# Performance work log

Hardware: AMD Instinct MI355X
Metric: run time of the kernel (lower is better)

The kernel has to match this reference:

```python
import jax, jax.numpy as jnp
import numpy as np

WEIGHT_GROUP = 128  # in-channel group size for scales (module default)


def setup_inputs() -> dict:
    key = jax.random.key(0)
    k1, k2, k3, k4, k5 = jax.random.split(key, 5)
    B, IN, OUT = 16, 8192, 8192
    nG = IN // WEIGHT_GROUP  # 64 scale groups along in_features
    x = jax.random.normal(k1, (B, IN), dtype=jnp.float32)
    # 'weight' stores the already-quantized low-bit float values (small magnitudes)
    weight = jax.random.normal(k2, (OUT, IN), dtype=jnp.float32)
    # per-(row, group) positive scales
    scale_buf = jax.random.uniform(k3, (OUT, nG), dtype=jnp.float32, minval=0.01, maxval=1.0)
    bias = jax.random.normal(k4, (1, OUT), dtype=jnp.float32)
    # per-[64, group]-block mantissa-format ids in {0,1,2}; selects the dequant
    # format on hardware but is a constant lookup (no float math) in the reference
    types = jax.random.randint(k5, (OUT // 64, nG), 0, 3, dtype=jnp.int32)
    return {"x": x, "weight": weight, "scale_buf": scale_buf, "bias": bias, "types": types}


def reference(x, weight, scale_buf, bias, types):
    O, I = weight.shape
    nG = scale_buf.shape[1]
    G = I // nG
    # group-wise dequant: w_deq[o, g*G + j] = weight[o, g*G + j] * scale_buf[o, g]
    w_deq = (weight.reshape(O, nG, G) * scale_buf[:, :, None]).reshape(O, I)
    # y = x @ W_deq^T + bias   [B, O]
    return jnp.einsum("bi,oi->bo", x, w_deq) + bias
```

## Files before the change

### kernel.cpp

```cpp
#include <hip/hip_runtime.h>

#define IN_F 8192
#define OUT_F 8192
#define NBATCH 16
#define KC 512
#define NG 64
#define KSPLIT 2
#define KRANGE (IN_F / KSPLIT)

__global__ __launch_bounds__(256)
void init_out_kernel(const float* __restrict__ bias, float* __restrict__ out) {
    const int i = blockIdx.x * 256 + threadIdx.x;
    out[i] = bias[i & (OUT_F - 1)];
}

__global__ __launch_bounds__(256, 4)
void axcore_dsew_linear_kernel(const float* __restrict__ x,
                               const float* __restrict__ w,
                               const float* __restrict__ scale,
                               float* __restrict__ out) {
    __shared__ __align__(16) float xlds[NBATCH * KC];

    const int t    = threadIdx.x;
    const int wv   = __builtin_amdgcn_readfirstlane(t >> 6);
    const int lane = t & 63;
    const int o0   = blockIdx.x * 16 + wv * 4;
    const int k0   = blockIdx.y * KRANGE;

    float acc[4][NBATCH];
#pragma unroll
    for (int r = 0; r < 4; ++r)
#pragma unroll
        for (int b = 0; b < NBATCH; ++b) acc[r][b] = 0.f;

    for (int kc = k0; kc < k0 + KRANGE; kc += KC) {
        __syncthreads();

        float4 wq[2][4];
#pragma unroll
        for (int s = 0; s < 2; ++s)
#pragma unroll
            for (int r = 0; r < 4; ++r)
                wq[s][r] = *(const float4*)&w[(size_t)(o0 + r) * IN_F + kc + s * 256 + 4 * lane];

        const int g0 = kc >> 7;
        float sc[2][4];
#pragma unroll
        for (int s = 0; s < 2; ++s)
#pragma unroll
            for (int r = 0; r < 4; ++r) {
                const float sa = scale[(o0 + r) * NG + g0 + 2 * s];
                const float sb = scale[(o0 + r) * NG + g0 + 2 * s + 1];
                sc[s][r] = (lane < 32) ? sa : sb;
            }

#pragma unroll
        for (int p = 0; p < 8; ++p) {
            const int fidx = p * 256 + t;
            const int bb = fidx >> 7;
            const int kq = fidx & 127;
            *(float4*)&xlds[bb * KC + 4 * kq] =
                *(const float4*)&x[bb * IN_F + kc + 4 * kq];
        }
        __syncthreads();

#pragma unroll
        for (int s = 0; s < 2; ++s) {
            const int klocal = s * 256 + 4 * lane;
            float4 wr[4];
#pragma unroll
            for (int r = 0; r < 4; ++r) {
                wr[r].x = wq[s][r].x * sc[s][r];
                wr[r].y = wq[s][r].y * sc[s][r];
                wr[r].z = wq[s][r].z * sc[s][r];
                wr[r].w = wq[s][r].w * sc[s][r];
            }
#pragma unroll
            for (int b = 0; b < NBATCH; ++b) {
                const float4 xv = *(const float4*)&xlds[b * KC + klocal];
#pragma unroll
                for (int r = 0; r < 4; ++r) {
                    acc[r][b] += wr[r].x * xv.x;
                    acc[r][b] += wr[r].y * xv.y;
                    acc[r][b] += wr[r].z * xv.z;
                    acc[r][b] += wr[r].w * xv.w;
                }
            }
        }
    }

#pragma unroll
    for (int r = 0; r < 4; ++r) {
        const int o = o0 + r;
#pragma unroll
        for (int b = 0; b < NBATCH; ++b) {
            float v = acc[r][b];
            v += __shfl_xor(v, 1);
            v += __shfl_xor(v, 2);
            v += __shfl_xor(v, 4);
            v += __shfl_xor(v, 8);
            v += __shfl_xor(v, 16);
            v += __shfl_xor(v, 32);
            if (lane == 0) atomicAdd(&out[b * OUT_F + o], v);
        }
    }
}

extern "C" void kernel_launch(void* const* d_in, const int* in_sizes, int n_in,
                              void* d_out, int out_size, void* d_ws, size_t ws_size,
                              hipStream_t stream) {
    const float* x    = (const float*)d_in[0];
    const float* w    = (const float*)d_in[1];
    const float* sc   = (const float*)d_in[2];
    const float* bias = (const float*)d_in[3];
    float* out = (float*)d_out;

    hipLaunchKernelGGL(init_out_kernel, dim3(NBATCH * OUT_F / 256), dim3(256),
                       0, stream, bias, out);
    hipLaunchKernelGGL(axcore_dsew_linear_kernel, dim3(OUT_F / 16, KSPLIT), dim3(256),
                       0, stream, x, w, sc, out);
}
```

Baseline: 445.6 us.

## Use bf16 MFMA for dequantized GEMV with wider K-split

New measurement: 403.0 us. 9.6% less time.

```diff
diff --git a/kernel.cpp b/kernel.cpp
--- a/kernel.cpp
+++ b/kernel.cpp
@@ -1,12 +1,21 @@
 #include <hip/hip_runtime.h>
+#include <hip/hip_bf16.h>
 
 #define IN_F 8192
 #define OUT_F 8192
-#define NBATCH 16
-#define KC 512
+#define NB 16
 #define NG 64
-#define KSPLIT 2
+#define KSPLIT 8
 #define KRANGE (IN_F / KSPLIT)
+#define NSTEP (KRANGE / 32)
+
+typedef __attribute__((ext_vector_type(8))) short bf16x8;
+typedef __attribute__((ext_vector_type(4))) float f32x4;
+
+static __device__ __forceinline__ short f2bf(float f) {
+    __hip_bfloat16 h = __float2bfloat16(f);
+    return *reinterpret_cast<short*>(&h);
+}
 
 __global__ __launch_bounds__(256)
 void init_out_kernel(const float* __restrict__ bias, float* __restrict__ out) {
@@ -15,94 +24,77 @@
 }
 
 __global__ __launch_bounds__(256, 4)
-void axcore_dsew_linear_kernel(const float* __restrict__ x,
-                               const float* __restrict__ w,
-                               const float* __restrict__ scale,
-                               float* __restrict__ out) {
-    __shared__ __align__(16) float xlds[NBATCH * KC];
+void axcore_mfma_kernel(const float* __restrict__ x,
+                        const float* __restrict__ w,
+                        const float* __restrict__ scale,
+                        float* __restrict__ out) {
+    __shared__ __align__(16) unsigned short xswz[NSTEP * 64 * 8];
 
     const int t    = threadIdx.x;
-    const int wv   = __builtin_amdgcn_readfirstlane(t >> 6);
+    const int wv   = t >> 6;
     const int lane = t & 63;
-    const int o0   = blockIdx.x * 16 + wv * 4;
     const int k0   = blockIdx.y * KRANGE;
-
-    float acc[4][NBATCH];
-#pragma unroll
-    for (int r = 0; r < 4; ++r)
-#pragma unroll
-        for (int b = 0; b < NBATCH; ++b) acc[r][b] = 0.f;
-
-    for (int kc = k0; kc < k0 + KRANGE; kc += KC) {
-        __syncthreads();
-
-        float4 wq[2][4];
-#pragma unroll
-        for (int s = 0; s < 2; ++s)
-#pragma unroll
-            for (int r = 0; r < 4; ++r)
-                wq[s][r] = *(const float4*)&w[(size_t)(o0 + r) * IN_F + kc + s * 256 + 4 * lane];
-
-        const int g0 = kc >> 7;
-        float sc[2][4];
-#pragma unroll
-        for (int s = 0; s < 2; ++s)
-#pragma unroll
-            for (int r = 0; r < 4; ++r) {
-                const float sa = scale[(o0 + r) * NG + g0 + 2 * s];
-                const float sb = scale[(o0 + r) * NG + g0 + 2 * s + 1];
-                sc[s][r] = (lane < 32) ? sa : sb;
-            }
+    const int o0   = blockIdx.x * 64 + wv * 16;
 
 #pragma unroll
-        for (int p = 0; p < 8; ++p) {
-            const int fidx = p * 256 + t;
-            const int bb = fidx >> 7;
-            const int kq = fidx & 127;
-            *(float4*)&xlds[bb * KC + 4 * kq] =
-                *(const float4*)&x[bb * IN_F + kc + 4 * kq];
-        }
-        __syncthreads();
+    for (int p = 0; p < 16; ++p) {
+        const int idx = p * 256 + t;
+        const int m   = idx >> 8;
+        const int k4  = (idx & 255) * 4;
+        const float4 v = *(const float4*)&x[m * IN_F + k0 + k4];
+        const int tt = k4 >> 5;
+        const int ln = m + 16 * ((k4 & 31) >> 3);
+        const int jj = k4 & 7;
+        ushort4 sv;
+        sv.x = (unsigned short)f2bf(v.x);
+        sv.y = (unsigned short)f2bf(v.y);
+        sv.z = (unsigned short)f2bf(v.z);
+        sv.w = (unsigned short)f2bf(v.w);
+        *(ushort4*)&xswz[(tt * 64 + ln) * 8 + jj] = sv;
+    }
+    __syncthreads();
 
+    const int nrow = o0 + (lane & 15);
+    const int koct = (lane >> 4) * 8;
+    const float* wrow = &w[(size_t)nrow * IN_F];
+
+    const float4 sA = *(const float4*)&scale[nrow * NG + (k0 >> 7)];
+    const float4 sB = *(const float4*)&scale[nrow * NG + (k0 >> 7) + 4];
+    float sg[8] = {sA.x, sA.y, sA.z, sA.w, sB.x, sB.y, sB.z, sB.w};
+
+    f32x4 acc = {0.f, 0.f, 0.f, 0.f};
+
+#pragma unroll 2
+    for (int gi = 0; gi < KRANGE / 128; ++gi) {
+        const float s = sg[gi];
 #pragma unroll
-        for (int s = 0; s < 2; ++s) {
-            const int klocal = s * 256 + 4 * lane;
-            float4 wr[4];
-#pragma unroll
-            for (int r = 0; r < 4; ++r) {
-                wr[r].x = wq[s][r].x * sc[s][r];
-                wr[r].y = wq[s][r].y * sc[s][r];
-                wr[r].z = wq[s][r].z * sc[s][r];
-                wr[r].w = wq[s][r].w * sc[s][r];
-            }
-#pragma unroll
-            for (int b = 0; b < NBATCH; ++b) {
-                const float4 xv = *(const float4*)&xlds[b * KC + klocal];
-#pragma unroll
-                for (int r = 0; r < 4; ++r) {
-                    acc[r][b] += wr[r].x * xv.x;
-                    acc[r][b] += wr[r].y * xv.y;
-                    acc[r][b] += wr[r].z * xv.z;
-                    acc[r][b] += wr[r].w * xv.w;
-                }
-            }
+        for (int ts = 0; ts < 4; ++ts) {
+            const int tt = gi * 4 + ts;
+            const int kg = k0 + tt * 32 + koct;
+            const float4 w0 = *(const float4*)&wrow[kg];
+            const float4 w1 = *(const float4*)&wrow[kg + 4];
+
+            bf16x8 bfrag;
+            bfrag[0] = f2bf(w0.x * s);
+            bfrag[1] = f2bf(w0.y * s);
+            bfrag[2] = f2bf(w0.z * s);
+            bfrag[3] = f2bf(w0.w * s);
+            bfrag[4] = f2bf(w1.x * s);
+            bfrag[5] = f2bf(w1.y * s);
+            bfrag[6] = f2bf(w1.z * s);
+            bfrag[7] = f2bf(w1.w * s);
+
+            const bf16x8 afrag = *(const bf16x8*)&xswz[(tt * 64 + lane) * 8];
+
+            acc = __builtin_amdgcn_mfma_f32_16x16x32_bf16(afrag, bfrag, acc,
+                                                          0, 0, 0);
         }
     }
 
 #pragma unroll
     for (int r = 0; r < 4; ++r) {
-        const int o = o0 + r;
-#pragma unroll
-        for (int b = 0; b < NBATCH; ++b) {
-            float v = acc[r][b];
-            v += __shfl_xor(v, 1);
-            v += __shfl_xor(v, 2);
-            v += __shfl_xor(v, 4);
-            v += __shfl_xor(v, 8);
-            v += __shfl_xor(v, 16);
-            v += __shfl_xor(v, 32);
-            if (lane == 0) atomicAdd(&out[b * OUT_F + o], v);
-        }
+        const int b = (lane >> 4) * 4 + r;
+        atomicAdd(&out[b * OUT_F + nrow], acc[r]);
     }
 }
 
@@ -115,8 +107,8 @@
     const float* bias = (const float*)d_in[3];
     float* out = (float*)d_out;
 
-    hipLaunchKernelGGL(init_out_kernel, dim3(NBATCH * OUT_F / 256), dim3(256),
+    hipLaunchKernelGGL(init_out_kernel, dim3(NB * OUT_F / 256), dim3(256),
                        0, stream, bias, out);
-    hipLaunchKernelGGL(axcore_dsew_linear_kernel, dim3(OUT_F / 16, KSPLIT), dim3(256),
+    hipLaunchKernelGGL(axcore_mfma_kernel, dim3(OUT_F / 64, KSPLIT), dim3(256),
                        0, stream, x, w, sc, out);
 }
```
